# Optimization experiments

Hardware: AMD Instinct MI355X
Metric: run time of the kernel (lower is better)

## Reference

```python
import jax, jax.numpy as jnp
import numpy as np

T, B, D, H, O = 64, 64, 512, 512, 128

def setup_inputs() -> dict:
    key = jax.random.key(0)
    ks = jax.random.split(key, 8)
    s = 0.05
    return {
        "x": jax.random.normal(ks[0], (T, B, D), jnp.float32),
        "w_ih": jax.random.normal(ks[1], (T, 4 * H, D), jnp.float32) * s,
        "w_hh": jax.random.normal(ks[2], (T, 4 * H, H), jnp.float32) * s,
        "b_ih": jax.random.normal(ks[3], (T, 4 * H), jnp.float32) * s,
        "b_hh": jax.random.normal(ks[4], (T, 4 * H), jnp.float32) * s,
        "w_ho": jax.random.normal(ks[5], (O, H), jnp.float32) * s,
        "b_ho": jax.random.normal(ks[6], (O,), jnp.float32) * s,
        "lengths": jax.random.randint(ks[7], (B,), 1, T + 1, jnp.int64 if jax.config.jax_enable_x64 else jnp.int32),
    }

def _lstm_scan(x, w_ih, w_hh, b_ih, b_hh):
    bs = x.shape[1]
    h0 = jnp.zeros((bs, H), x.dtype)
    c0 = jnp.zeros((bs, H), x.dtype)

    def step(carry, inp):
        h, c = carry
        xt, Wih, Whh, bih, bhh = inp
        # gates: [B, 4H], torch gate order i, f, g, o
        gates = xt @ Wih.T + bih + h @ Whh.T + bhh
        i, f, g, o = jnp.split(gates, 4, axis=-1)
        c = jax.nn.sigmoid(f) * c + jax.nn.sigmoid(i) * jnp.tanh(g)
        h = jax.nn.sigmoid(o) * jnp.tanh(c)
        return (h, c), h

    (_, _), outs = jax.lax.scan(step, (h0, c0), (x, w_ih, w_hh, b_ih, b_hh))
    return outs  # [T, B, H]

def reference(x, w_ih, w_hh, b_ih, b_hh, w_ho, b_ho, lengths):
    outs = _lstm_scan(x, w_ih, w_hh, b_ih, b_hh)
    bs = x.shape[1]
    h_t = outs[lengths - 1, jnp.arange(bs)]  # [B, H] last valid output per seq
    logits = h_t @ w_ho.T + b_ho
    return jax.nn.log_softmax(logits, axis=1)
```

## Files before the change

kernel.cpp:

```cpp
#include <hip/hip_runtime.h>
#include <math.h>

#define TT 64
#define BB 64
#define DD 512
#define HH 512
#define G4 2048
#define OO 128

typedef unsigned short us16;
typedef __attribute__((ext_vector_type(8))) short bf16x8;
typedef __attribute__((ext_vector_type(4))) float f32x4;
typedef __attribute__((ext_vector_type(4))) unsigned u32x4;

__device__ __forceinline__ unsigned pk_bf16(float lo, float hi) {
  unsigned r;
  asm volatile("v_cvt_pk_bf16_f32 %0, %1, %2" : "=v"(r) : "v"(lo), "v"(hi));
  return r;
}

__device__ __forceinline__ float sigm(float v) { return 1.f / (1.f + expf(-v)); }
__device__ __forceinline__ float fsigm(float v) { return 1.f / (1.f + __expf(-v)); }
__device__ __forceinline__ float ftanh(float v) { return 1.f - 2.f / (__expf(2.f * v) + 1.f); }

__device__ __forceinline__ u32x4 load_b128_cc(const void* p) {
  u32x4 r;
  asm volatile("global_load_dwordx4 %0, %1, off sc0 sc1" : "=v"(r) : "v"(p));
  return r;
}
__device__ __forceinline__ void store_b128_cc(void* p, u32x4 v) {
  asm volatile("global_store_dwordx4 %0, %1, off sc0 sc1" ::"v"(p), "v"(v) : "memory");
}

__global__ __launch_bounds__(256) void phaseA_mfma(
    const float* __restrict__ x, const float* __restrict__ wih,
    const float* __restrict__ bih, const float* __restrict__ bhh,
    float* __restrict__ Gb) {
  __shared__ us16 xa[2][64][64];
  __shared__ us16 wbuf[2][128][64];
  const int tid = threadIdx.x;
  const int t = blockIdx.y;
  const int j0 = blockIdx.x * 128;
  const int wv = tid >> 6, lane = tid & 63;
  const int wm = wv & 1, wn = wv >> 1;
  const float* xb = x + (size_t)t * (BB * DD);
  const float* wg = wih + (size_t)t * (G4 * DD) + (size_t)j0 * DD;

  float4 xr[2][2], wr[4][2];
  int xrow[2], xc[2], wrow[4], wc[4];
#pragma unroll
  for (int i = 0; i < 2; i++) { int cid = tid + i * 256; xrow[i] = cid >> 3; xc[i] = cid & 7; }
#pragma unroll
  for (int i = 0; i < 4; i++) { int cid = tid + i * 256; wrow[i] = cid >> 3; wc[i] = cid & 7; }

  auto loadx = [&](int k0) {
#pragma unroll
    for (int i = 0; i < 2; i++) {
      const float* p = xb + xrow[i] * DD + k0 + xc[i] * 8;
      xr[i][0] = *(const float4*)p; xr[i][1] = *(const float4*)(p + 4);
    }
  };
  auto loadw = [&](int k0) {
#pragma unroll
    for (int i = 0; i < 4; i++) {
      const float* p = wg + (size_t)wrow[i] * DD + k0 + wc[i] * 8;
      wr[i][0] = *(const float4*)p; wr[i][1] = *(const float4*)(p + 4);
    }
  };
  auto store = [&](int buf) {
#pragma unroll
    for (int i = 0; i < 2; i++) {
      uint4 u;
      u.x = pk_bf16(xr[i][0].x, xr[i][0].y); u.y = pk_bf16(xr[i][0].z, xr[i][0].w);
      u.z = pk_bf16(xr[i][1].x, xr[i][1].y); u.w = pk_bf16(xr[i][1].z, xr[i][1].w);
      int p = xc[i] ^ (xrow[i] & 7);
      *(uint4*)&xa[buf][xrow[i]][p * 8] = u;
    }
#pragma unroll
    for (int i = 0; i < 4; i++) {
      uint4 u;
      u.x = pk_bf16(wr[i][0].x, wr[i][0].y); u.y = pk_bf16(wr[i][0].z, wr[i][0].w);
      u.z = pk_bf16(wr[i][1].x, wr[i][1].y); u.w = pk_bf16(wr[i][1].z, wr[i][1].w);
      int p = wc[i] ^ (wrow[i] & 7);
      *(uint4*)&wbuf[buf][wrow[i]][p * 8] = u;
    }
  };

  loadx(0); loadw(0); store(0);
  __syncthreads();

  f32x4 zero = {0.f, 0.f, 0.f, 0.f};
  f32x4 acc[2][4];
#pragma unroll
  for (int mt = 0; mt < 2; mt++)
#pragma unroll
    for (int nt = 0; nt < 4; nt++) acc[mt][nt] = zero;

  for (int s = 0; s < 8; s++) {
    const int nb = s & 1;
    if (s < 7) { loadx((s + 1) * 64); loadw((s + 1) * 64); }
#pragma unroll
    for (int ks = 0; ks < 2; ks++) {
      const int cc = ks * 4 + (lane >> 4);
      bf16x8 a[2], b[4];
#pragma unroll
      for (int mt = 0; mt < 2; mt++) {
        int r = wm * 32 + mt * 16 + (lane & 15);
        a[mt] = *(const bf16x8*)&xa[nb][r][(cc ^ (r & 7)) * 8];
      }
#pragma unroll
      for (int nt = 0; nt < 4; nt++) {
        int r = wn * 64 + nt * 16 + (lane & 15);
        b[nt] = *(const bf16x8*)&wbuf[nb][r][(cc ^ (r & 7)) * 8];
      }
#pragma unroll
      for (int mt = 0; mt < 2; mt++)
#pragma unroll
        for (int nt = 0; nt < 4; nt++)
          acc[mt][nt] = __builtin_amdgcn_mfma_f32_16x16x32_bf16(a[mt], b[nt], acc[mt][nt], 0, 0, 0);
    }
    __syncthreads();
    if (s < 7) store(nb ^ 1);
    __syncthreads();
  }

  float bias[4]; int jn[4];
#pragma unroll
  for (int nt = 0; nt < 4; nt++) {
    jn[nt] = j0 + wn * 64 + nt * 16 + (lane & 15);
    bias[nt] = bih[t * G4 + jn[nt]] + bhh[t * G4 + jn[nt]];
  }
#pragma unroll
  for (int mt = 0; mt < 2; mt++)
#pragma unroll
    for (int nt = 0; nt < 4; nt++)
#pragma unroll
      for (int e = 0; e < 4; e++) {
        int brow = wm * 32 + mt * 16 + (lane >> 4) * 4 + e;
        Gb[((size_t)t * BB + brow) * G4 + jn[nt]] = acc[mt][nt][e] + bias[nt];
      }
}

__global__ __launch_bounds__(256, 1) void lstm_persist(
    const float* __restrict__ whh, const float* __restrict__ Gb,
    const int* __restrict__ lengths, char* __restrict__ hb,
    float* __restrict__ hf) {
  __shared__ float gm[2][16][36];

  const int tid = threadIdx.x, bid = blockIdx.x;
  const int bh = bid & 1, ug = bid >> 1;
  const int wv = tid >> 6, lane = tid & 63;
  const int wm = wv & 1, kq = wv >> 1;
  const int l15 = lane & 15, klg = lane >> 4;

  const size_t jrow = (size_t)((l15 >> 2) * 512 + ug * 4 + (l15 & 3));

  float4 pf[8][2];
  auto prefW = [&](int tt) {
    const float* wt = whh + (size_t)tt * (G4 * HH) + jrow * HH;
#pragma unroll
    for (int s = 0; s < 8; s++) {
      const float* p = wt + (size_t)(kq * 32 + s * 4 + klg) * 8;
      pf[s][0] = *(const float4*)p;
      pf[s][1] = *(const float4*)(p + 4);
    }
  };
  bf16x8 wfrag[8];
  auto cvtW = [&]() {
#pragma unroll
    for (int s = 0; s < 8; s++) {
      uint4 u;
      u.x = pk_bf16(pf[s][0].x, pf[s][0].y); u.y = pk_bf16(pf[s][0].z, pf[s][0].w);
      u.z = pk_bf16(pf[s][1].x, pf[s][1].y); u.w = pk_bf16(pf[s][1].z, pf[s][1].w);
      wfrag[s] = __builtin_bit_cast(bf16x8, u);
    }
  };

  float2 gpre[4];
  auto prefG = [&](int tt) {
    if (wv == 0) {
      const float* gbp =
          Gb + ((size_t)tt * BB + bh * 32 + (lane & 31)) * G4 + ug * 4 + ((lane >> 5) << 1);
#pragma unroll
      for (int q = 0; q < 4; q++) gpre[q] = *(const float2*)(gbp + q * 512);
    }
  };

  const size_t cbase =
      (size_t)bh * 65536 + ((size_t)(kq * 64 + klg * 2) * 32 + wm * 16 + l15) * 16;
  const size_t pbase = (size_t)bh * 65536 + ((size_t)ug * 32 + (lane & 31)) * 16;

  const int mylen = (wv == 0) ? lengths[bh * 32 + (lane & 31)] : -2;
  float cst[2] = {0.f, 0.f};

  prefW(0);
  prefG(0);

  for (int t = 0; t < TT; t++) {
    cvtW();

    u32x4 r0[8], r1[8];
    if (t == 0) {
      u32x4 z = {0u, 0u, 0u, 0u};
#pragma unroll
      for (int s = 0; s < 8; s++) { r0[s] = z; r1[s] = z; }
    } else {
      const char* sbase = hb + (size_t)(t & 1) * 131072 + cbase;
      const unsigned tg = (unsigned)t;
      bool ok;
      do {
#pragma unroll
        for (int s = 0; s < 8; s++) {
          r0[s] = load_b128_cc(sbase + (size_t)s * 4096);
          r1[s] = load_b128_cc(sbase + (size_t)s * 4096 + 512);
        }
        asm volatile("s_waitcnt vmcnt(0)" ::: "memory");
        __builtin_amdgcn_sched_barrier(0);
        ok = true;
#pragma unroll
        for (int s = 0; s < 8; s++) ok = ok && (r0[s].z == tg) && (r1[s].z == tg);
        if (!__all(ok)) {
          __builtin_amdgcn_s_sleep(1);
          ok = false;
        } else {
          ok = true;
        }
      } while (!ok);
    }

    f32x4 acc = {0.f, 0.f, 0.f, 0.f};
#pragma unroll
    for (int s = 0; s < 8; s++) {
      u32x4 fa;
      fa.x = r0[s].x; fa.y = r0[s].y; fa.z = r1[s].x; fa.w = r1[s].y;
      acc = __builtin_amdgcn_mfma_f32_16x16x32_bf16(__builtin_bit_cast(bf16x8, fa),
                                                    wfrag[s], acc, 0, 0, 0);
    }
    *(f32x4*)&gm[kq][l15][wm * 16 + klg * 4] = acc;

    __syncthreads();

    float2 gcur[4];
    if (wv == 0) {
#pragma unroll
      for (int q = 0; q < 4; q++) gcur[q] = gpre[q];
    }
    if (t + 1 < TT) { prefW(t + 1); prefG(t + 1); }

    if (wv == 0) {
      const int b = lane & 31, hi = lane >> 5;
      float hv[2];
#pragma unroll
      for (int uu = 0; uu < 2; uu++) {
        const int lu = hi * 2 + uu;
        float vi = (uu ? gcur[0].y : gcur[0].x) + gm[0][0 + lu][b] + gm[1][0 + lu][b];
        float vf = (uu ? gcur[1].y : gcur[1].x) + gm[0][4 + lu][b] + gm[1][4 + lu][b];
        float vg = (uu ? gcur[2].y : gcur[2].x) + gm[0][8 + lu][b] + gm[1][8 + lu][b];
        float vo = (uu ? gcur[3].y : gcur[3].x) + gm[0][12 + lu][b] + gm[1][12 + lu][b];
        float cn = fsigm(vf) * cst[uu] + fsigm(vi) * ftanh(vg);
        cst[uu] = cn;
        hv[uu] = fsigm(vo) * ftanh(cn);
      }
      unsigned hw = pk_bf16(hv[0], hv[1]);
      unsigned other = __shfl_xor(hw, 32);
      if (hi == 0 && t + 1 < TT) {
        u32x4 rec;
        rec.x = hw; rec.y = other; rec.z = (unsigned)(t + 1); rec.w = 0u;
        store_b128_cc(hb + (size_t)((t + 1) & 1) * 131072 + pbase, rec);
      }
      if (mylen - 1 == t) {
        float2 o2; o2.x = hv[0]; o2.y = hv[1];
        *(float2*)&hf[(size_t)(bh * 32 + b) * HH + ug * 4 + hi * 2] = o2;
      }
    }
  }
}

__global__ __launch_bounds__(128) void finalK(const float* __restrict__ hf,
                                              const float* __restrict__ who,
                                              const float* __restrict__ bho,
                                              float* __restrict__ out) {
  int b = blockIdx.x, o = threadIdx.x;
  const float* h = hf + b * HH;
  const float* w = who + o * HH;
  float s = bho[o];
#pragma unroll 4
  for (int k = 0; k < HH; k += 4) {
    float4 hv = *(const float4*)(h + k);
    float4 wv = *(const float4*)(w + k);
    s += hv.x * wv.x + hv.y * wv.y + hv.z * wv.z + hv.w * wv.w;
  }
  __shared__ float red[2];
  __shared__ float red2[2];
  float m = s;
#pragma unroll
  for (int msk = 32; msk; msk >>= 1) m = fmaxf(m, __shfl_xor(m, msk));
  int wave = o >> 6;
  if ((o & 63) == 0) red[wave] = m;
  __syncthreads();
  m = fmaxf(red[0], red[1]);
  float e = expf(s - m);
#pragma unroll
  for (int msk = 32; msk; msk >>= 1) e += __shfl_xor(e, msk);
  if ((o & 63) == 0) red2[wave] = e;
  __syncthreads();
  float sum = red2[0] + red2[1];
  out[b * OO + o] = (s - m) - logf(sum);
}

extern "C" void kernel_launch(void* const* d_in, const int* in_sizes, int n_in,
                              void* d_out, int out_size, void* d_ws, size_t ws_size,
                              hipStream_t stream) {
  const float* x = (const float*)d_in[0];
  const float* wih = (const float*)d_in[1];
  const float* whh = (const float*)d_in[2];
  const float* bih = (const float*)d_in[3];
  const float* bhh = (const float*)d_in[4];
  const float* who = (const float*)d_in[5];
  const float* bho = (const float*)d_in[6];
  const int* lengths = (const int*)d_in[7];
  float* out = (float*)d_out;

  char* ws = (char*)d_ws;
  float* Gb = (float*)ws;
  char* hb = ws + 33554432;
  float* hf = (float*)(ws + 33554432 + 262144);

  (void)hipMemsetAsync(hb, 0, 262144, stream);

  phaseA_mfma<<<dim3(16, 64), 256, 0, stream>>>(x, wih, bih, bhh, Gb);
  lstm_persist<<<256, 256, 0, stream>>>(whh, Gb, lengths, hb, hf);
  finalK<<<BB, 128, 0, stream>>>(hf, who, bho, out);
}
```

Before: 341.8 us.

## Add producer wavefront to prefetch W_hh into LDS ahead of recurrent steps

The persistent LSTM kernel gains a fifth wavefront that streams the per-timestep W_hh slice from global memory two steps ahead, converts it to bf16 and writes it into a double-buffered, XOR-swizzled LDS tile. The four compute wavefronts then read their MFMA B-fragments from LDS instead of holding prefetched fp32 registers and converting them on the critical path. The MFMA at t=0 is skipped because h is zero. This takes weight loads and conversions off the serial recurrence and frees registers in the compute waves, in exchange for 32KB of LDS, larger blocks, and the producer's participation in every step's __syncthreads.

```diff
diff --git a/kernel.cpp b/kernel.cpp
--- a/kernel.cpp
+++ b/kernel.cpp
@@ -19,7 +19,6 @@
   return r;
 }
 
-__device__ __forceinline__ float sigm(float v) { return 1.f / (1.f + expf(-v)); }
 __device__ __forceinline__ float fsigm(float v) { return 1.f / (1.f + __expf(-v)); }
 __device__ __forceinline__ float ftanh(float v) { return 1.f - 2.f / (__expf(2.f * v) + 1.f); }
 
@@ -141,137 +140,155 @@
       }
 }
 
-__global__ __launch_bounds__(256, 1) void lstm_persist(
+__global__ __launch_bounds__(320, 1) void lstm_persist(
     const float* __restrict__ whh, const float* __restrict__ Gb,
     const int* __restrict__ lengths, char* __restrict__ hb,
     float* __restrict__ hf) {
+  __shared__ us16 wbuf[2][16][512];
   __shared__ float gm[2][16][36];
 
   const int tid = threadIdx.x, bid = blockIdx.x;
   const int bh = bid & 1, ug = bid >> 1;
   const int wv = tid >> 6, lane = tid & 63;
-  const int wm = wv & 1, kq = wv >> 1;
   const int l15 = lane & 15, klg = lane >> 4;
 
-  const size_t jrow = (size_t)((l15 >> 2) * 512 + ug * 4 + (l15 & 3));
-
-  float4 pf[8][2];
-  auto prefW = [&](int tt) {
-    const float* wt = whh + (size_t)tt * (G4 * HH) + jrow * HH;
-#pragma unroll
-    for (int s = 0; s < 8; s++) {
-      const float* p = wt + (size_t)(kq * 32 + s * 4 + klg) * 8;
-      pf[s][0] = *(const float4*)p;
-      pf[s][1] = *(const float4*)(p + 4);
-    }
-  };
-  bf16x8 wfrag[8];
-  auto cvtW = [&]() {
-#pragma unroll
-    for (int s = 0; s < 8; s++) {
-      uint4 u;
-      u.x = pk_bf16(pf[s][0].x, pf[s][0].y); u.y = pk_bf16(pf[s][0].z, pf[s][0].w);
-      u.z = pk_bf16(pf[s][1].x, pf[s][1].y); u.w = pk_bf16(pf[s][1].z, pf[s][1].w);
-      wfrag[s] = __builtin_bit_cast(bf16x8, u);
-    }
-  };
-
-  float2 gpre[4];
-  auto prefG = [&](int tt) {
-    if (wv == 0) {
-      const float* gbp =
-          Gb + ((size_t)tt * BB + bh * 32 + (lane & 31)) * G4 + ug * 4 + ((lane >> 5) << 1);
-#pragma unroll
-      for (int q = 0; q < 4; q++) gpre[q] = *(const float2*)(gbp + q * 512);
-    }
-  };
-
-  const size_t cbase =
-      (size_t)bh * 65536 + ((size_t)(kq * 64 + klg * 2) * 32 + wm * 16 + l15) * 16;
-  const size_t pbase = (size_t)bh * 65536 + ((size_t)ug * 32 + (lane & 31)) * 16;
-
-  const int mylen = (wv == 0) ? lengths[bh * 32 + (lane & 31)] : -2;
-  float cst[2] = {0.f, 0.f};
-
-  prefW(0);
-  prefG(0);
-
-  for (int t = 0; t < TT; t++) {
-    cvtW();
-
-    u32x4 r0[8], r1[8];
-    if (t == 0) {
-      u32x4 z = {0u, 0u, 0u, 0u};
-#pragma unroll
-      for (int s = 0; s < 8; s++) { r0[s] = z; r1[s] = z; }
-    } else {
-      const char* sbase = hb + (size_t)(t & 1) * 131072 + cbase;
-      const unsigned tg = (unsigned)t;
-      bool ok;
-      do {
+  if (wv < 4) {
+    const int wm = wv & 1, kq = wv >> 1;
+
+    float2 gpre[4];
+    auto prefG = [&](int tt) {
+      if (wv == 0) {
+        const float* gbp =
+            Gb + ((size_t)tt * BB + bh * 32 + (lane & 31)) * G4 + ug * 4 + ((lane >> 5) << 1);
+#pragma unroll
+        for (int q = 0; q < 4; q++) gpre[q] = *(const float2*)(gbp + q * 512);
+      }
+    };
+
+    const size_t cbase =
+        (size_t)bh * 65536 + ((size_t)(kq * 64 + klg * 2) * 32 + wm * 16 + l15) * 16;
+    const size_t pbase = (size_t)bh * 65536 + ((size_t)ug * 32 + (lane & 31)) * 16;
+
+    const int mylen = (wv == 0) ? lengths[bh * 32 + (lane & 31)] : -2;
+    float cst[2] = {0.f, 0.f};
+
+    prefG(0);
+
+    for (int t = 0; t < TT; t++) {
+      f32x4 acc = {0.f, 0.f, 0.f, 0.f};
+      if (t > 0) {
+        u32x4 r0[8], r1[8];
+        const char* sbase = hb + (size_t)(t & 1) * 131072 + cbase;
+        const unsigned tg = (unsigned)t;
+        bool ok;
+        do {
+#pragma unroll
+          for (int s = 0; s < 8; s++) {
+            r0[s] = load_b128_cc(sbase + (size_t)s * 4096);
+            r1[s] = load_b128_cc(sbase + (size_t)s * 4096 + 512);
+          }
+          asm volatile("s_waitcnt vmcnt(0)" ::: "memory");
+          __builtin_amdgcn_sched_barrier(0);
+          ok = true;
+#pragma unroll
+          for (int s = 0; s < 8; s++) ok = ok && (r0[s].z == tg) && (r1[s].z == tg);
+          if (!__all(ok)) {
+            __builtin_amdgcn_s_sleep(1);
+            ok = false;
+          } else {
+            ok = true;
+          }
+        } while (!ok);
+
+        bf16x8 wf[8];
 #pragma unroll
         for (int s = 0; s < 8; s++) {
-          r0[s] = load_b128_cc(sbase + (size_t)s * 4096);
-          r1[s] = load_b128_cc(sbase + (size_t)s * 4096 + 512);
-        }
-        asm volatile("s_waitcnt vmcnt(0)" ::: "memory");
-        __builtin_amdgcn_sched_barrier(0);
-        ok = true;
-#pragma unroll
-        for (int s = 0; s < 8; s++) ok = ok && (r0[s].z == tg) && (r1[s].z == tg);
-        if (!__all(ok)) {
-          __builtin_amdgcn_s_sleep(1);
-          ok = false;
-        } else {
-          ok = true;
-        }
-      } while (!ok);
-    }
-
-    f32x4 acc = {0.f, 0.f, 0.f, 0.f};
-#pragma unroll
-    for (int s = 0; s < 8; s++) {
-      u32x4 fa;
-      fa.x = r0[s].x; fa.y = r0[s].y; fa.z = r1[s].x; fa.w = r1[s].y;
-      acc = __builtin_amdgcn_mfma_f32_16x16x32_bf16(__builtin_bit_cast(bf16x8, fa),
-                                                    wfrag[s], acc, 0, 0, 0);
-    }
-    *(f32x4*)&gm[kq][l15][wm * 16 + klg * 4] = acc;
-
-    __syncthreads();
-
-    float2 gcur[4];
-    if (wv == 0) {
-#pragma unroll
-      for (int q = 0; q < 4; q++) gcur[q] = gpre[q];
-    }
-    if (t + 1 < TT) { prefW(t + 1); prefG(t + 1); }
-
-    if (wv == 0) {
-      const int b = lane & 31, hi = lane >> 5;
-      float hv[2];
-#pragma unroll
-      for (int uu = 0; uu < 2; uu++) {
-        const int lu = hi * 2 + uu;
-        float vi = (uu ? gcur[0].y : gcur[0].x) + gm[0][0 + lu][b] + gm[1][0 + lu][b];
-        float vf = (uu ? gcur[1].y : gcur[1].x) + gm[0][4 + lu][b] + gm[1][4 + lu][b];
-        float vg = (uu ? gcur[2].y : gcur[2].x) + gm[0][8 + lu][b] + gm[1][8 + lu][b];
-        float vo = (uu ? gcur[3].y : gcur[3].x) + gm[0][12 + lu][b] + gm[1][12 + lu][b];
-        float cn = fsigm(vf) * cst[uu] + fsigm(vi) * ftanh(vg);
-        cst[uu] = cn;
-        hv[uu] = fsigm(vo) * ftanh(cn);
-      }
-      unsigned hw = pk_bf16(hv[0], hv[1]);
-      unsigned other = __shfl_xor(hw, 32);
-      if (hi == 0 && t + 1 < TT) {
-        u32x4 rec;
-        rec.x = hw; rec.y = other; rec.z = (unsigned)(t + 1); rec.w = 0u;
-        store_b128_cc(hb + (size_t)((t + 1) & 1) * 131072 + pbase, rec);
-      }
-      if (mylen - 1 == t) {
-        float2 o2; o2.x = hv[0]; o2.y = hv[1];
-        *(float2*)&hf[(size_t)(bh * 32 + b) * HH + ug * 4 + hi * 2] = o2;
-      }
+          int cc = kq * 32 + s * 4 + klg;
+          wf[s] = *(const bf16x8*)&wbuf[t & 1][l15][(cc ^ (l15 & 7)) * 8];
+        }
+#pragma unroll
+        for (int s = 0; s < 8; s++) {
+          u32x4 fa;
+          fa.x = r0[s].x; fa.y = r0[s].y; fa.z = r1[s].x; fa.w = r1[s].y;
+          acc = __builtin_amdgcn_mfma_f32_16x16x32_bf16(__builtin_bit_cast(bf16x8, fa),
+                                                        wf[s], acc, 0, 0, 0);
+        }
+      }
+      *(f32x4*)&gm[kq][l15][wm * 16 + klg * 4] = acc;
+
+      __syncthreads();
+
+      float2 gcur[4];
+      if (wv == 0) {
+#pragma unroll
+        for (int q = 0; q < 4; q++) gcur[q] = gpre[q];
+      }
+      if (t + 1 < TT) prefG(t + 1);
+
+      if (wv == 0) {
+        const int b = lane & 31, hi = lane >> 5;
+        float hv[2];
+#pragma unroll
+        for (int uu = 0; uu < 2; uu++) {
+          const int lu = hi * 2 + uu;
+          float vi = (uu ? gcur[0].y : gcur[0].x) + gm[0][0 + lu][b] + gm[1][0 + lu][b];
+          float vf = (uu ? gcur[1].y : gcur[1].x) + gm[0][4 + lu][b] + gm[1][4 + lu][b];
+          float vg = (uu ? gcur[2].y : gcur[2].x) + gm[0][8 + lu][b] + gm[1][8 + lu][b];
+          float vo = (uu ? gcur[3].y : gcur[3].x) + gm[0][12 + lu][b] + gm[1][12 + lu][b];
+          float cn = fsigm(vf) * cst[uu] + fsigm(vi) * ftanh(vg);
+          cst[uu] = cn;
+          hv[uu] = fsigm(vo) * ftanh(cn);
+        }
+        unsigned hw = pk_bf16(hv[0], hv[1]);
+        unsigned other = __shfl_xor(hw, 32);
+        if (hi == 0 && t + 1 < TT) {
+          u32x4 rec;
+          rec.x = hw; rec.y = other; rec.z = (unsigned)(t + 1); rec.w = 0u;
+          store_b128_cc(hb + (size_t)((t + 1) & 1) * 131072 + pbase, rec);
+        }
+        if (mylen - 1 == t) {
+          float2 o2; o2.x = hv[0]; o2.y = hv[1];
+          *(float2*)&hf[(size_t)(bh * 32 + b) * HH + ug * 4 + hi * 2] = o2;
+        }
+      }
+    }
+  } else {
+    const int jr = lane >> 2, cq = lane & 3;
+    const size_t srow = (size_t)((jr >> 2) * 512 + ug * 4 + (jr & 3)) * HH;
+    float4 pA[32], pB[32];
+
+    auto issueTo = [&](int tt, float4 (&p)[32]) {
+      const float* wt = whh + (size_t)tt * (G4 * HH) + srow;
+#pragma unroll
+      for (int i = 0; i < 16; i++) {
+        const float* q = wt + (size_t)(cq + i * 4) * 8;
+        p[2 * i] = *(const float4*)q;
+        p[2 * i + 1] = *(const float4*)(q + 4);
+      }
+    };
+    auto writeFrom = [&](int slot, float4 (&p)[32]) {
+#pragma unroll
+      for (int i = 0; i < 16; i++) {
+        int ci = cq + i * 4;
+        u32x4 w;
+        w.x = pk_bf16(p[2 * i].x, p[2 * i].y);
+        w.y = pk_bf16(p[2 * i].z, p[2 * i].w);
+        w.z = pk_bf16(p[2 * i + 1].x, p[2 * i + 1].y);
+        w.w = pk_bf16(p[2 * i + 1].z, p[2 * i + 1].w);
+        *(u32x4*)&wbuf[slot][jr][(ci ^ (jr & 7)) * 8] = w;
+      }
+    };
+
+    issueTo(1, pA);
+    for (int t = 0; t < TT; t++) {
+      if (t & 1) {
+        if (t + 2 < TT) issueTo(t + 2, pA);
+        if (t + 1 < TT) writeFrom((t + 1) & 1, pB);
+      } else {
+        if (t + 2 < TT) issueTo(t + 2, pB);
+        if (t + 1 < TT) writeFrom((t + 1) & 1, pA);
+      }
+      __syncthreads();
     }
   }
 }
@@ -329,6 +346,6 @@
   (void)hipMemsetAsync(hb, 0, 262144, stream);
 
   phaseA_mfma<<<dim3(16, 64), 256, 0, stream>>>(x, wih, bih, bhh, Gb);
-  lstm_persist<<<256, 256, 0, stream>>>(whh, Gb, lengths, hb, hf);
+  lstm_persist<<<256, 320, 0, stream>>>(whh, Gb, lengths, hb, hf);
   finalK<<<BB, 128, 0, stream>>>(hf, who, bho, out);
 }
```

Result: slower. 949.8 us (+177.8%).

## Fuse input projection and persistent recurrence into one launch with per-step counters

Applied to the files above, without the earlier changes.

Merges the input-projection GEMM and the persistent LSTM recurrence into a single kernel. The first 1024 blocks compute the gate pre-activations and bump a per-timestep counter once their stores are visible. The last 256 blocks run the recurrence and spin on those counters two steps ahead, so the recurrence can start before the whole projection is done and one launch gap goes away. The trade-offs are a lower per-block register budget from launch_bounds(256,2), coherent-cache stores for the gate buffer, and reliance on block dispatch order for forward progress.

```diff
diff --git a/kernel.cpp b/kernel.cpp
--- a/kernel.cpp
+++ b/kernel.cpp
@@ -19,7 +19,6 @@
   return r;
 }
 
-__device__ __forceinline__ float sigm(float v) { return 1.f / (1.f + expf(-v)); }
 __device__ __forceinline__ float fsigm(float v) { return 1.f / (1.f + __expf(-v)); }
 __device__ __forceinline__ float ftanh(float v) { return 1.f - 2.f / (__expf(2.f * v) + 1.f); }
 
@@ -31,125 +30,133 @@
 __device__ __forceinline__ void store_b128_cc(void* p, u32x4 v) {
   asm volatile("global_store_dwordx4 %0, %1, off sc0 sc1" ::"v"(p), "v"(v) : "memory");
 }
-
-__global__ __launch_bounds__(256) void phaseA_mfma(
+__device__ __forceinline__ void store_b32_cc(void* p, float vf) {
+  unsigned v = __builtin_bit_cast(unsigned, vf);
+  asm volatile("global_store_dword %0, %1, off sc0 sc1" ::"v"(p), "v"(v) : "memory");
+}
+
+__global__ __launch_bounds__(256, 2) void fused_lstm(
     const float* __restrict__ x, const float* __restrict__ wih,
     const float* __restrict__ bih, const float* __restrict__ bhh,
-    float* __restrict__ Gb) {
+    const float* __restrict__ whh, float* __restrict__ Gb,
+    const int* __restrict__ lengths, char* __restrict__ hb,
+    float* __restrict__ hf, unsigned* __restrict__ gcnt) {
   __shared__ us16 xa[2][64][64];
-  __shared__ us16 wbuf[2][128][64];
-  const int tid = threadIdx.x;
-  const int t = blockIdx.y;
-  const int j0 = blockIdx.x * 128;
+  __shared__ us16 wbufA[2][128][64];
+  __shared__ float gm[2][16][36];
+
+  const int tid = threadIdx.x, bid = blockIdx.x;
   const int wv = tid >> 6, lane = tid & 63;
-  const int wm = wv & 1, wn = wv >> 1;
-  const float* xb = x + (size_t)t * (BB * DD);
-  const float* wg = wih + (size_t)t * (G4 * DD) + (size_t)j0 * DD;
-
-  float4 xr[2][2], wr[4][2];
-  int xrow[2], xc[2], wrow[4], wc[4];
-#pragma unroll
-  for (int i = 0; i < 2; i++) { int cid = tid + i * 256; xrow[i] = cid >> 3; xc[i] = cid & 7; }
-#pragma unroll
-  for (int i = 0; i < 4; i++) { int cid = tid + i * 256; wrow[i] = cid >> 3; wc[i] = cid & 7; }
-
-  auto loadx = [&](int k0) {
-#pragma unroll
-    for (int i = 0; i < 2; i++) {
-      const float* p = xb + xrow[i] * DD + k0 + xc[i] * 8;
-      xr[i][0] = *(const float4*)p; xr[i][1] = *(const float4*)(p + 4);
-    }
-  };
-  auto loadw = [&](int k0) {
-#pragma unroll
-    for (int i = 0; i < 4; i++) {
-      const float* p = wg + (size_t)wrow[i] * DD + k0 + wc[i] * 8;
-      wr[i][0] = *(const float4*)p; wr[i][1] = *(const float4*)(p + 4);
-    }
-  };
-  auto store = [&](int buf) {
-#pragma unroll
-    for (int i = 0; i < 2; i++) {
-      uint4 u;
-      u.x = pk_bf16(xr[i][0].x, xr[i][0].y); u.y = pk_bf16(xr[i][0].z, xr[i][0].w);
-      u.z = pk_bf16(xr[i][1].x, xr[i][1].y); u.w = pk_bf16(xr[i][1].z, xr[i][1].w);
-      int p = xc[i] ^ (xrow[i] & 7);
-      *(uint4*)&xa[buf][xrow[i]][p * 8] = u;
-    }
-#pragma unroll
-    for (int i = 0; i < 4; i++) {
-      uint4 u;
-      u.x = pk_bf16(wr[i][0].x, wr[i][0].y); u.y = pk_bf16(wr[i][0].z, wr[i][0].w);
-      u.z = pk_bf16(wr[i][1].x, wr[i][1].y); u.w = pk_bf16(wr[i][1].z, wr[i][1].w);
-      int p = wc[i] ^ (wrow[i] & 7);
-      *(uint4*)&wbuf[buf][wrow[i]][p * 8] = u;
-    }
-  };
-
-  loadx(0); loadw(0); store(0);
-  __syncthreads();
-
-  f32x4 zero = {0.f, 0.f, 0.f, 0.f};
-  f32x4 acc[2][4];
-#pragma unroll
-  for (int mt = 0; mt < 2; mt++)
-#pragma unroll
-    for (int nt = 0; nt < 4; nt++) acc[mt][nt] = zero;
-
-  for (int s = 0; s < 8; s++) {
-    const int nb = s & 1;
-    if (s < 7) { loadx((s + 1) * 64); loadw((s + 1) * 64); }
-#pragma unroll
-    for (int ks = 0; ks < 2; ks++) {
-      const int cc = ks * 4 + (lane >> 4);
-      bf16x8 a[2], b[4];
-#pragma unroll
-      for (int mt = 0; mt < 2; mt++) {
-        int r = wm * 32 + mt * 16 + (lane & 15);
-        a[mt] = *(const bf16x8*)&xa[nb][r][(cc ^ (r & 7)) * 8];
-      }
-#pragma unroll
-      for (int nt = 0; nt < 4; nt++) {
-        int r = wn * 64 + nt * 16 + (lane & 15);
-        b[nt] = *(const bf16x8*)&wbuf[nb][r][(cc ^ (r & 7)) * 8];
-      }
-#pragma unroll
-      for (int mt = 0; mt < 2; mt++)
-#pragma unroll
-        for (int nt = 0; nt < 4; nt++)
-          acc[mt][nt] = __builtin_amdgcn_mfma_f32_16x16x32_bf16(a[mt], b[nt], acc[mt][nt], 0, 0, 0);
-    }
+
+  if (bid < 1024) {
+    const int t = bid >> 4;
+    const int j0 = (bid & 15) * 128;
+    const int wm = wv & 1, wn = wv >> 1;
+    const float* xb = x + (size_t)t * (BB * DD);
+    const float* wg = wih + (size_t)t * (G4 * DD) + (size_t)j0 * DD;
+
+    float4 xr[2][2], wr[4][2];
+    int xrow[2], xc[2], wrow[4], wc[4];
+#pragma unroll
+    for (int i = 0; i < 2; i++) { int cid = tid + i * 256; xrow[i] = cid >> 3; xc[i] = cid & 7; }
+#pragma unroll
+    for (int i = 0; i < 4; i++) { int cid = tid + i * 256; wrow[i] = cid >> 3; wc[i] = cid & 7; }
+
+    auto loadx = [&](int k0) {
+#pragma unroll
+      for (int i = 0; i < 2; i++) {
+        const float* p = xb + xrow[i] * DD + k0 + xc[i] * 8;
+        xr[i][0] = *(const float4*)p; xr[i][1] = *(const float4*)(p + 4);
+      }
+    };
+    auto loadw = [&](int k0) {
+#pragma unroll
+      for (int i = 0; i < 4; i++) {
+        const float* p = wg + (size_t)wrow[i] * DD + k0 + wc[i] * 8;
+        wr[i][0] = *(const float4*)p; wr[i][1] = *(const float4*)(p + 4);
+      }
+    };
+    auto store = [&](int buf) {
+#pragma unroll
+      for (int i = 0; i < 2; i++) {
+        uint4 u;
+        u.x = pk_bf16(xr[i][0].x, xr[i][0].y); u.y = pk_bf16(xr[i][0].z, xr[i][0].w);
+        u.z = pk_bf16(xr[i][1].x, xr[i][1].y); u.w = pk_bf16(xr[i][1].z, xr[i][1].w);
+        int p = xc[i] ^ (xrow[i] & 7);
+        *(uint4*)&xa[buf][xrow[i]][p * 8] = u;
+      }
+#pragma unroll
+      for (int i = 0; i < 4; i++) {
+        uint4 u;
+        u.x = pk_bf16(wr[i][0].x, wr[i][0].y); u.y = pk_bf16(wr[i][0].z, wr[i][0].w);
+        u.z = pk_bf16(wr[i][1].x, wr[i][1].y); u.w = pk_bf16(wr[i][1].z, wr[i][1].w);
+        int p = wc[i] ^ (wrow[i] & 7);
+        *(uint4*)&wbufA[buf][wrow[i]][p * 8] = u;
+      }
+    };
+
+    loadx(0); loadw(0); store(0);
     __syncthreads();
-    if (s < 7) store(nb ^ 1);
+
+    f32x4 zero = {0.f, 0.f, 0.f, 0.f};
+    f32x4 acc[2][4];
+#pragma unroll
+    for (int mt = 0; mt < 2; mt++)
+#pragma unroll
+      for (int nt = 0; nt < 4; nt++) acc[mt][nt] = zero;
+
+    for (int s = 0; s < 8; s++) {
+      const int nb = s & 1;
+      if (s < 7) { loadx((s + 1) * 64); loadw((s + 1) * 64); }
+#pragma unroll
+      for (int ks = 0; ks < 2; ks++) {
+        const int cc = ks * 4 + (lane >> 4);
+        bf16x8 a[2], b[4];
+#pragma unroll
+        for (int mt = 0; mt < 2; mt++) {
+          int r = wm * 32 + mt * 16 + (lane & 15);
+          a[mt] = *(const bf16x8*)&xa[nb][r][(cc ^ (r & 7)) * 8];
+        }
+#pragma unroll
+        for (int nt = 0; nt < 4; nt++) {
+          int r = wn * 64 + nt * 16 + (lane & 15);
+          b[nt] = *(const bf16x8*)&wbufA[nb][r][(cc ^ (r & 7)) * 8];
+        }
+#pragma unroll
+        for (int mt = 0; mt < 2; mt++)
+#pragma unroll
+          for (int nt = 0; nt < 4; nt++)
+            acc[mt][nt] = __builtin_amdgcn_mfma_f32_16x16x32_bf16(a[mt], b[nt], acc[mt][nt], 0, 0, 0);
+      }
+      __syncthreads();
+      if (s < 7) store(nb ^ 1);
+      __syncthreads();
+    }
+
+    float bias[4]; int jn[4];
+#pragma unroll
+    for (int nt = 0; nt < 4; nt++) {
+      jn[nt] = j0 + wn * 64 + nt * 16 + (lane & 15);
+      bias[nt] = bih[t * G4 + jn[nt]] + bhh[t * G4 + jn[nt]];
+    }
+#pragma unroll
+    for (int mt = 0; mt < 2; mt++)
+#pragma unroll
+      for (int nt = 0; nt < 4; nt++)
+#pragma unroll
+        for (int e = 0; e < 4; e++) {
+          int brow = wm * 32 + mt * 16 + (lane >> 4) * 4 + e;
+          store_b32_cc(&Gb[((size_t)t * BB + brow) * G4 + jn[nt]], acc[mt][nt][e] + bias[nt]);
+        }
+    asm volatile("s_waitcnt vmcnt(0)" ::: "memory");
     __syncthreads();
+    if (tid == 0)
+      __hip_atomic_fetch_add(&gcnt[t], 1u, __ATOMIC_RELAXED, __HIP_MEMORY_SCOPE_AGENT);
+    return;
   }
 
-  float bias[4]; int jn[4];
-#pragma unroll
-  for (int nt = 0; nt < 4; nt++) {
-    jn[nt] = j0 + wn * 64 + nt * 16 + (lane & 15);
-    bias[nt] = bih[t * G4 + jn[nt]] + bhh[t * G4 + jn[nt]];
-  }
-#pragma unroll
-  for (int mt = 0; mt < 2; mt++)
-#pragma unroll
-    for (int nt = 0; nt < 4; nt++)
-#pragma unroll
-      for (int e = 0; e < 4; e++) {
-        int brow = wm * 32 + mt * 16 + (lane >> 4) * 4 + e;
-        Gb[((size_t)t * BB + brow) * G4 + jn[nt]] = acc[mt][nt][e] + bias[nt];
-      }
-}
-
-__global__ __launch_bounds__(256, 1) void lstm_persist(
-    const float* __restrict__ whh, const float* __restrict__ Gb,
-    const int* __restrict__ lengths, char* __restrict__ hb,
-    float* __restrict__ hf) {
-  __shared__ float gm[2][16][36];
-
-  const int tid = threadIdx.x, bid = blockIdx.x;
-  const int bh = bid & 1, ug = bid >> 1;
-  const int wv = tid >> 6, lane = tid & 63;
+  const int lbid = bid - 1024;
+  const int bh = lbid & 1, ug = lbid >> 1;
   const int wm = wv & 1, kq = wv >> 1;
   const int l15 = lane & 15, klg = lane >> 4;
 
@@ -185,6 +192,10 @@
       for (int q = 0; q < 4; q++) gpre[q] = *(const float2*)(gbp + q * 512);
     }
   };
+  auto gate = [&](int tt) {
+    while (__hip_atomic_load(&gcnt[tt], __ATOMIC_RELAXED, __HIP_MEMORY_SCOPE_AGENT) < 16u)
+      __builtin_amdgcn_s_sleep(8);
+  };
 
   const size_t cbase =
       (size_t)bh * 65536 + ((size_t)(kq * 64 + klg * 2) * 32 + wm * 16 + l15) * 16;
@@ -194,6 +205,8 @@
   float cst[2] = {0.f, 0.f};
 
   prefW(0);
+  if (wv == 2) { gate(0); gate(1); }
+  __syncthreads();
   prefG(0);
 
   for (int t = 0; t < TT; t++) {
@@ -245,6 +258,7 @@
 #pragma unroll
       for (int q = 0; q < 4; q++) gcur[q] = gpre[q];
     }
+    if (wv == 2 && t + 2 < TT) gate(t + 2);
     if (t + 1 < TT) { prefW(t + 1); prefG(t + 1); }
 
     if (wv == 0) {
@@ -324,11 +338,11 @@
   char* ws = (char*)d_ws;
   float* Gb = (float*)ws;
   char* hb = ws + 33554432;
-  float* hf = (float*)(ws + 33554432 + 262144);
-
-  (void)hipMemsetAsync(hb, 0, 262144, stream);
-
-  phaseA_mfma<<<dim3(16, 64), 256, 0, stream>>>(x, wih, bih, bhh, Gb);
-  lstm_persist<<<256, 256, 0, stream>>>(whh, Gb, lengths, hb, hf);
+  unsigned* gcnt = (unsigned*)(ws + 33554432 + 262144);
+  float* hf = (float*)(ws + 33554432 + 262400);
+
+  (void)hipMemsetAsync(hb, 0, 262400, stream);
+
+  fused_lstm<<<1280, 256, 0, stream>>>(x, wih, bih, bhh, whh, Gb, lengths, hb, hf, gcnt);
   finalK<<<BB, 128, 0, stream>>>(hf, who, bho, out);
 }
```

Result: slower. 491.7 us (+43.8%).

## Embed step parity tag in bf16 hidden-state bits to halve exchange traffic

Applied to the files above, without the earlier changes.

Replaces the 16-byte record (two packed bf16 words plus a step tag) with a single 32-bit store per lane. The step parity is encoded in bit 14 of each bf16 half, so readers spin on dense 16-byte loads that are pure payload and then mask the tag bit off before the MFMA. This halves the exchange buffer and the number of polling loads per step, and removes the cross-lane shuffle. In exchange it relies on bit 14 of every bf16 value being known (set or clear) for the tag to work; masking with 0xBFFF clears that bit, so any h value whose real bit 14 was set gets corrupted, and magnitudes at or above 2 cannot survive. A second memset initialises the alternate buffer's tags.

```diff
diff --git a/kernel.cpp b/kernel.cpp
--- a/kernel.cpp
+++ b/kernel.cpp
@@ -19,7 +19,6 @@
   return r;
 }
 
-__device__ __forceinline__ float sigm(float v) { return 1.f / (1.f + expf(-v)); }
 __device__ __forceinline__ float fsigm(float v) { return 1.f / (1.f + __expf(-v)); }
 __device__ __forceinline__ float ftanh(float v) { return 1.f - 2.f / (__expf(2.f * v) + 1.f); }
 
@@ -28,8 +27,8 @@
   asm volatile("global_load_dwordx4 %0, %1, off sc0 sc1" : "=v"(r) : "v"(p));
   return r;
 }
-__device__ __forceinline__ void store_b128_cc(void* p, u32x4 v) {
-  asm volatile("global_store_dwordx4 %0, %1, off sc0 sc1" ::"v"(p), "v"(v) : "memory");
+__device__ __forceinline__ void store_b32u_cc(void* p, unsigned v) {
+  asm volatile("global_store_dword %0, %1, off sc0 sc1" ::"v"(p), "v"(v) : "memory");
 }
 
 __global__ __launch_bounds__(256) void phaseA_mfma(
@@ -152,6 +151,7 @@
   const int wv = tid >> 6, lane = tid & 63;
   const int wm = wv & 1, kq = wv >> 1;
   const int l15 = lane & 15, klg = lane >> 4;
+  const unsigned M = 0x40004000u;
 
   const size_t jrow = (size_t)((l15 >> 2) * 512 + ug * 4 + (l15 & 3));
 
@@ -187,8 +187,10 @@
   };
 
   const size_t cbase =
-      (size_t)bh * 65536 + ((size_t)(kq * 64 + klg * 2) * 32 + wm * 16 + l15) * 16;
-  const size_t pbase = (size_t)bh * 65536 + ((size_t)ug * 32 + (lane & 31)) * 16;
+      (size_t)bh * 32768 + ((size_t)(kq * 32 + klg) * 32 + wm * 16 + l15) * 16;
+  const size_t pbase = (size_t)bh * 32768 +
+                       ((size_t)(ug >> 1) * 32 + (lane & 31)) * 16 +
+                       (size_t)((ug * 2 + (lane >> 5)) & 3) * 4;
 
   const int mylen = (wv == 0) ? lengths[bh * 32 + (lane & 31)] : -2;
   float cst[2] = {0.f, 0.f};
@@ -199,43 +201,42 @@
   for (int t = 0; t < TT; t++) {
     cvtW();
 
-    u32x4 r0[8], r1[8];
+    u32x4 r[8];
     if (t == 0) {
       u32x4 z = {0u, 0u, 0u, 0u};
 #pragma unroll
-      for (int s = 0; s < 8; s++) { r0[s] = z; r1[s] = z; }
+      for (int s = 0; s < 8; s++) r[s] = z;
     } else {
-      const char* sbase = hb + (size_t)(t & 1) * 131072 + cbase;
-      const unsigned tg = (unsigned)t;
+      const char* sbase = hb + (size_t)(t & 1) * 65536 + cbase;
+      const unsigned tw = ((t >> 1) & 1) ? M : 0u;
       bool ok;
       do {
 #pragma unroll
-        for (int s = 0; s < 8; s++) {
-          r0[s] = load_b128_cc(sbase + (size_t)s * 4096);
-          r1[s] = load_b128_cc(sbase + (size_t)s * 4096 + 512);
-        }
+        for (int s = 0; s < 8; s++) r[s] = load_b128_cc(sbase + (size_t)s * 2048);
         asm volatile("s_waitcnt vmcnt(0)" ::: "memory");
         __builtin_amdgcn_sched_barrier(0);
-        ok = true;
-#pragma unroll
-        for (int s = 0; s < 8; s++) ok = ok && (r0[s].z == tg) && (r1[s].z == tg);
-        if (!__all(ok)) {
+        unsigned bad = 0u;
+#pragma unroll
+        for (int s = 0; s < 8; s++) {
+          bad |= ((r[s].x & M) ^ tw) | ((r[s].y & M) ^ tw);
+          bad |= ((r[s].z & M) ^ tw) | ((r[s].w & M) ^ tw);
+        }
+        if (!__all(bad == 0u)) {
           __builtin_amdgcn_s_sleep(1);
           ok = false;
         } else {
           ok = true;
         }
       } while (!ok);
+#pragma unroll
+      for (int s = 0; s < 8; s++) r[s] &= 0xBFFFBFFFu;
     }
 
     f32x4 acc = {0.f, 0.f, 0.f, 0.f};
 #pragma unroll
-    for (int s = 0; s < 8; s++) {
-      u32x4 fa;
-      fa.x = r0[s].x; fa.y = r0[s].y; fa.z = r1[s].x; fa.w = r1[s].y;
-      acc = __builtin_amdgcn_mfma_f32_16x16x32_bf16(__builtin_bit_cast(bf16x8, fa),
+    for (int s = 0; s < 8; s++)
+      acc = __builtin_amdgcn_mfma_f32_16x16x32_bf16(__builtin_bit_cast(bf16x8, r[s]),
                                                     wfrag[s], acc, 0, 0, 0);
-    }
     *(f32x4*)&gm[kq][l15][wm * 16 + klg * 4] = acc;
 
     __syncthreads();
@@ -261,12 +262,10 @@
         cst[uu] = cn;
         hv[uu] = fsigm(vo) * ftanh(cn);
       }
-      unsigned hw = pk_bf16(hv[0], hv[1]);
-      unsigned other = __shfl_xor(hw, 32);
-      if (hi == 0 && t + 1 < TT) {
-        u32x4 rec;
-        rec.x = hw; rec.y = other; rec.z = (unsigned)(t + 1); rec.w = 0u;
-        store_b128_cc(hb + (size_t)((t + 1) & 1) * 131072 + pbase, rec);
+      if (t + 1 < TT) {
+        unsigned tagb = (((t + 1) >> 1) & 1) ? M : 0u;
+        unsigned hw = pk_bf16(hv[0], hv[1]) | tagb;
+        store_b32u_cc(hb + (size_t)((t + 1) & 1) * 65536 + pbase, hw);
       }
       if (mylen - 1 == t) {
         float2 o2; o2.x = hv[0]; o2.y = hv[1];
@@ -324,9 +323,10 @@
   char* ws = (char*)d_ws;
   float* Gb = (float*)ws;
   char* hb = ws + 33554432;
-  float* hf = (float*)(ws + 33554432 + 262144);
-
-  (void)hipMemsetAsync(hb, 0, 262144, stream);
+  float* hf = (float*)(ws + 33554432 + 131072);
+
+  (void)hipMemsetAsync(hb, 0x00, 65536, stream);
+  (void)hipMemsetAsync(hb + 65536, 0x40, 65536, stream);
 
   phaseA_mfma<<<dim3(16, 64), 256, 0, stream>>>(x, wih, bih, bhh, Gb);
   lstm_persist<<<256, 256, 0, stream>>>(whh, Gb, lengths, hb, hf);
```

After: 376.6 us. +10.2%, slower.
